# Performance work log

Measured on AMD Instinct MI355X. Metric: run time of the kernel, lower is better.

Reference implementation:

```python
import jax, jax.numpy as jnp
import numpy as np

R_MIN = 0.01
R_MAX = 0.6
H = 32            # polar radial bins (after pooling)
W = 64            # polar angular bins (after pooling)
UP_R = 10         # radial upsampling factor
UP_T = 10         # angular upsampling factor
ATT_ALPHA = 5.0
B, C, IMG = 64, 3, 224


def _conv(x, w, b):
    # NCHW valid conv, stride 1 (matches nn.Conv2d default padding=0)
    y = jax.lax.conv_general_dilated(x, w, (1, 1), 'VALID',
                                     dimension_numbers=('NCHW', 'OIHW', 'NCHW'))
    return y + b[None, :, None, None]


def _maxpool2(x):
    return jax.lax.reduce_window(x, -jnp.inf, jax.lax.max,
                                 (1, 1, 2, 2), (1, 1, 2, 2), 'VALID')


def _grid_sample_border(x, grid):
    # F.grid_sample, bilinear, padding_mode='border', align_corners=False
    Bn, Cn, Hi, Wi = x.shape
    ix = ((grid[..., 0] + 1.0) * Wi - 1.0) * 0.5   # x-coord -> width index
    iy = ((grid[..., 1] + 1.0) * Hi - 1.0) * 0.5   # y-coord -> height index
    x0f = jnp.floor(ix)
    y0f = jnp.floor(iy)
    wx = (ix - x0f)[..., None]
    wy = (iy - y0f)[..., None]
    x0 = jnp.clip(x0f.astype(jnp.int32), 0, Wi - 1)
    x1 = jnp.clip(x0f.astype(jnp.int32) + 1, 0, Wi - 1)
    y0 = jnp.clip(y0f.astype(jnp.int32), 0, Hi - 1)
    y1 = jnp.clip(y0f.astype(jnp.int32) + 1, 0, Hi - 1)
    bidx = jnp.arange(Bn)[:, None, None]
    v00 = x[bidx, :, y0, x0]   # [B,Hg,Wg,C]
    v01 = x[bidx, :, y0, x1]
    v10 = x[bidx, :, y1, x0]
    v11 = x[bidx, :, y1, x1]
    out = (v00 * (1 - wx) * (1 - wy) + v01 * wx * (1 - wy)
           + v10 * (1 - wx) * wy + v11 * wx * wy)
    return jnp.transpose(out, (0, 3, 1, 2))  # [B,C,Hg,Wg]


def setup_inputs() -> dict:
    key = jax.random.key(0)
    ks = jax.random.split(key, 10)
    x = jax.random.normal(ks[0], (B, C, IMG, IMG), dtype=jnp.float32)
    l_t_prev = jax.random.uniform(ks[1], (B, 2), dtype=jnp.float32)
    conv1_w = jax.random.normal(ks[2], (6, C, 5, 5), dtype=jnp.float32) * 0.1
    conv1_b = jnp.zeros((6,), jnp.float32)
    conv2_w = jax.random.normal(ks[3], (16, 6, 5, 5), dtype=jnp.float32) * 0.1
    conv2_b = jnp.zeros((16,), jnp.float32)
    fc1_w = jax.random.normal(ks[4], (8, 16), dtype=jnp.float32) * 0.1
    fc1_b = jnp.zeros((8,), jnp.float32)
    fc2_w = jax.random.normal(ks[5], (2, 8), dtype=jnp.float32) * 0.1
    fc2_b = jnp.zeros((2,), jnp.float32)
    return dict(x=x, l_t_prev=l_t_prev, conv1_w=conv1_w, conv1_b=conv1_b,
                conv2_w=conv2_w, conv2_b=conv2_b, fc1_w=fc1_w, fc1_b=fc1_b,
                fc2_w=fc2_w, fc2_b=fc2_b)


def reference(x, l_t_prev, conv1_w, conv1_b, conv2_w, conv2_b,
              fc1_w, fc1_b, fc2_w, fc2_b):
    # --- attention branch: conv -> maxpool -> conv -> GAP -> fc -> sigmoid ---
    h = _conv(x, conv1_w, conv1_b)
    h = _maxpool2(h)
    h = _conv(h, conv2_w, conv2_b)
    feat = h.mean(axis=(2, 3))                     # AdaptiveAvgPool2d(1), [B,16]
    h = jax.nn.relu(feat @ fc1_w.T + fc1_b)
    weight = jax.nn.sigmoid(h @ fc2_w.T + fc2_b) * ATT_ALPHA   # [B,2]
    # --- per-batch log-polar grid ---
    Hg, Wg = H * UP_R, W * UP_T
    angle = 2.0 * jnp.pi * jnp.arange(Wg, dtype=jnp.float32) / Wg
    unit = jnp.stack([jnp.sin(angle), jnp.cos(angle)], axis=-1)   # [Wg,2]
    start = jnp.log(R_MIN * weight[:, 0])
    stop = jnp.log(R_MAX * weight[:, 1])
    t = jnp.arange(Hg, dtype=jnp.float32) / (Hg - 1)
    radii = jnp.exp(start[:, None] + (stop - start)[:, None] * t[None])  # [B,Hg]
    grid = radii[:, :, None, None] * unit[None, None]     # [B,Hg,Wg,2]
    grid = grid + l_t_prev[:, None, None, :]
    # --- irregular bilinear sampling + box filter ---
    sampled = _grid_sample_border(x, grid)                 # [B,C,Hg,Wg]
    Bn, Cn = sampled.shape[:2]
    pooled = sampled.reshape(Bn, Cn, H, UP_R, W, UP_T).mean(axis=(3, 5))
    return pooled, weight
```

## Files before the change

kernel.cpp:

```cpp
#include <hip/hip_runtime.h>
#include <math.h>

#define Bn    64
#define Cn    3
#define IMG   224
#define PLANE (IMG*IMG)
#define C1    6
#define P1    110
#define P2    106
#define NVALID (P2*P2)
#define Hh    32
#define Ww    64
#define UPR   10
#define UPT   10
#define Hg    (Hh*UPR)
#define Wg    (Ww*UPT)
#define POOLED_SIZE (Bn*Cn*Hh*Ww)
#define RPB   4
#define NCHUNK ((P1 + RPB - 1) / RPB)
#define PSTRIDE 152

typedef unsigned short u16;
typedef float v2f __attribute__((ext_vector_type(2)));

#define PART_FLOATS ((size_t)Bn * NCHUNK * PSTRIDE)
#define X4B_U16     ((size_t)Bn * PLANE * 4)
#define WS_NEEDED   ((PART_FLOATS + Bn * 2) * 4 + X4B_U16 * 2)

__device__ __forceinline__ u16 f2bf(float f) {
    union { unsigned int u; float f; } c; c.f = f;
    unsigned int r = c.u + 0x7fffu + ((c.u >> 16) & 1u);
    return (u16)(r >> 16);
}
__device__ __forceinline__ float bf2f(u16 v) {
    union { unsigned int u; float f; } c; c.u = ((unsigned int)v) << 16;
    return c.f;
}

__device__ __forceinline__ void load_pairs(v2f* P, const float* rp) {
    const float4 a = *(const float4*)rp;
    const float4 c = *(const float4*)(rp + 4);
    P[0] = (v2f){a.x, a.y};
    P[1] = (v2f){a.y, a.z};
    P[2] = (v2f){a.z, a.w};
    P[3] = (v2f){a.w, c.x};
    P[4] = (v2f){c.x, c.y};
    P[5] = (v2f){c.y, c.z};
    P[6] = (v2f){c.z, c.w};
}

__global__ __launch_bounds__(256) void k1_fused(
    const float* __restrict__ x,
    const float* __restrict__ w1,
    const float* __restrict__ b1,
    float* __restrict__ partial,
    u16* __restrict__ x4b,
    int do_pack)
{
    __shared__ __attribute__((aligned(16))) float xs[3][12][224];
    __shared__ float psum[RPB][PSTRIDE];

    const int b    = blockIdx.y;
    const int tid  = threadIdx.x;
    const int wid  = tid >> 6;
    const int lane = tid & 63;

    const float* xb = x + (size_t)b * (Cn * PLANE);

    for (int half = 0; half < 2; ++half) {
        const int chunk = 2 * blockIdx.x + half;
        const int y0 = chunk * RPB;
        const int gybase = 2 * y0;

        for (int i = tid; i < 3 * 12 * 56; i += 256) {
            const int ic  = i / (12 * 56);
            const int rem = i - ic * (12 * 56);
            const int r   = rem / 56;
            const int c4  = rem - r * 56;
            const int gy  = gybase + r;
            if (gy < IMG)
                *(float4*)(&xs[ic][r][c4 * 4]) =
                    *(const float4*)(xb + ic * PLANE + gy * IMG + c4 * 4);
        }
        __syncthreads();

        if (do_pack) {
            u16* ob = x4b + (size_t)b * PLANE * 4;
            for (int i = tid; i < 8 * IMG; i += 256) {
                const int r   = i / IMG;
                const int col = i - r * IMG;
                const int gy  = gybase + r;
                ushort4 v;
                v.x = f2bf(xs[0][r][col]);
                v.y = f2bf(xs[1][r][col]);
                v.z = f2bf(xs[2][r][col]);
                v.w = 0;
                *(ushort4*)(ob + ((size_t)gy * IMG + col) * 4) = v;
            }
        }

        const int y = y0 + wid;
        const bool rowvalid = (y < P1);
        const bool active = (lane < 55) && rowvalid;

        float pp0[C1], pp1[C1];
        if (active) {
            v2f accT01[C1], accT23[C1], accB01[C1], accB23[C1];
            #pragma unroll
            for (int oc = 0; oc < C1; ++oc) {
                const float bv = b1[oc];
                const v2f bvv = (v2f){bv, bv};
                accT01[oc] = bvv; accT23[oc] = bvv;
                accB01[oc] = bvv; accB23[oc] = bvv;
            }

            #pragma unroll
            for (int ic = 0; ic < 3; ++ic) {
                v2f Pa[7], Pb[7];
                load_pairs(Pa, &xs[ic][2 * wid][4 * lane]);
                load_pairs(Pb, &xs[ic][2 * wid + 1][4 * lane]);
                #pragma unroll
                for (int ky = 0; ky < 5; ++ky) {
                    const v2f* Pt = (ky & 1) ? Pb : Pa;
                    const v2f* Po = (ky & 1) ? Pa : Pb;
                    #pragma unroll
                    for (int oc = 0; oc < C1; ++oc) {
                        const float* wrow = w1 + ((oc * 3 + ic) * 25 + ky * 5);
                        #pragma unroll
                        for (int kx = 0; kx < 5; ++kx) {
                            const float wv = wrow[kx];
                            const v2f wvv = (v2f){wv, wv};
                            accT01[oc] += Pt[kx]     * wvv;
                            accT23[oc] += Pt[kx + 2] * wvv;
                            accB01[oc] += Po[kx]     * wvv;
                            accB23[oc] += Po[kx + 2] * wvv;
                        }
                    }
                    if (ky < 4)
                        load_pairs((ky & 1) ? Pb : Pa,
                                   &xs[ic][2 * wid + ky + 2][4 * lane]);
                }
            }

            #pragma unroll
            for (int oc = 0; oc < C1; ++oc) {
                pp0[oc] = fmaxf(fmaxf(accT01[oc].x, accT01[oc].y),
                                fmaxf(accB01[oc].x, accB01[oc].y));
                pp1[oc] = fmaxf(fmaxf(accT23[oc].x, accT23[oc].y),
                                fmaxf(accB23[oc].x, accB23[oc].y));
            }
        } else {
            #pragma unroll
            for (int oc = 0; oc < C1; ++oc) { pp0[oc] = 0.0f; pp1[oc] = 0.0f; }
        }

        #pragma unroll
        for (int oc = 0; oc < C1; ++oc) {
            float s = pp0[oc] + pp1[oc];
            #pragma unroll
            for (int off = 32; off > 0; off >>= 1) s += __shfl_xor(s, off, 64);
            const float c0   = __shfl(pp0[oc], 0, 64);
            const float c1   = __shfl(pp1[oc], 0, 64);
            const float c2   = __shfl(pp0[oc], 1, 64);
            const float c3   = __shfl(pp1[oc], 1, 64);
            const float c106 = __shfl(pp0[oc], 53, 64);
            const float c107 = __shfl(pp1[oc], 53, 64);
            const float c108 = __shfl(pp0[oc], 54, 64);
            const float c109 = __shfl(pp1[oc], 54, 64);
            const float w0v = s - (c106 + c107 + c108 + c109);
            const float w1v = s - c0 - (c107 + c108 + c109);
            const float w2v = s - (c0 + c1) - (c108 + c109);
            const float w3v = s - (c0 + c1 + c2) - c109;
            const float w4v = s - (c0 + c1 + c2 + c3);
            if (lane < 25) {
                const int ky = lane / 5;
                const int kx = lane % 5;
                float wv = w0v;
                wv = (kx == 1) ? w1v : wv;
                wv = (kx == 2) ? w2v : wv;
                wv = (kx == 3) ? w3v : wv;
                wv = (kx == 4) ? w4v : wv;
                const bool valid = rowvalid && ((unsigned)(y - ky) <= 105u);
                psum[wid][oc * 25 + lane] = valid ? wv : 0.0f;
            }
        }
        __syncthreads();

        if (tid < 150) {
            const float v = psum[0][tid] + psum[1][tid] + psum[2][tid] + psum[3][tid];
            partial[((size_t)b * NCHUNK + chunk) * PSTRIDE + tid] = v;
        }
    }
}

__global__ __launch_bounds__(256) void k2_head(
    const float* __restrict__ partial, const float* __restrict__ w2,
    const float* __restrict__ b2, const float* __restrict__ fc1w,
    const float* __restrict__ fc1b, const float* __restrict__ fc2w,
    const float* __restrict__ fc2b, float* __restrict__ wt_ws,
    float* __restrict__ out)
{
    const int b = blockIdx.x;
    const int tid = threadIdx.x;
    __shared__ float wsb[150];
    __shared__ float sfeat[16];
    __shared__ float sh[8];

    if (tid < 150) {
        const float* p = partial + (size_t)b * NCHUNK * PSTRIDE + tid;
        float s = 0.0f;
        #pragma unroll
        for (int c = 0; c < NCHUNK; ++c) s += p[c * PSTRIDE];
        wsb[tid] = s;
    }
    __syncthreads();
    if (tid < 16) {
        float s = 0.0f;
        for (int j = 0; j < 150; ++j) s += w2[tid * 150 + j] * wsb[j];
        sfeat[tid] = b2[tid] + s * (1.0f / (float)NVALID);
    }
    __syncthreads();
    if (tid < 8) {
        float s = fc1b[tid];
        #pragma unroll
        for (int j = 0; j < 16; ++j) s += fc1w[tid * 16 + j] * sfeat[j];
        sh[tid] = fmaxf(s, 0.0f);
    }
    __syncthreads();
    if (tid < 2) {
        float s = fc2b[tid];
        #pragma unroll
        for (int j = 0; j < 8; ++j) s += fc2w[tid * 8 + j] * sh[j];
        float sig = (s >= 0.0f) ? (1.0f / (1.0f + expf(-s)))
                                : (expf(s) / (1.0f + expf(s)));
        const float wgt = 5.0f * sig;
        wt_ws[b * 2 + tid] = wgt;
        out[POOLED_SIZE + b * 2 + tid] = wgt;
    }
}

__device__ __forceinline__ void sample_coords(
    float gxn, float gyn, int& x0, int& y0, float& wx, float& wy)
{
    float ix = ((gxn + 1.0f) * (float)IMG - 1.0f) * 0.5f;
    float iy = ((gyn + 1.0f) * (float)IMG - 1.0f) * 0.5f;
    ix = fminf(fmaxf(ix, 0.0f), (float)(IMG - 1));
    iy = fminf(fmaxf(iy, 0.0f), (float)(IMG - 1));
    x0 = (int)ix; if (x0 > IMG - 2) x0 = IMG - 2;
    y0 = (int)iy; if (y0 > IMG - 2) y0 = IMG - 2;
    wx = ix - (float)x0;
    wy = iy - (float)y0;
}

__global__ __launch_bounds__(640) void k3_sample_pool_bf16(
    const u16* __restrict__ x4b,
    const float* __restrict__ ltp,
    const float* __restrict__ wt,
    float* __restrict__ out)
{
    __shared__ float part[3 * Wg];

    const int L = blockIdx.x;
    const int q = L >> 3;
    const int h = q & 31;
    const int b = (L & 7) + 8 * (q >> 5);
    const int tid = threadIdx.x;

    const float w0 = wt[b * 2 + 0];
    const float w1 = wt[b * 2 + 1];
    const float l0 = ltp[b * 2 + 0];
    const float l1 = ltp[b * 2 + 1];
    const float start = logf(0.01f * w0);
    const float stop  = logf(0.6f  * w1);
    const float dr = stop - start;

    const float angle = 6.283185307179586f * (float)tid / (float)Wg;
    const float sn = sinf(angle);
    const float cs = cosf(angle);

    const u16* xb4 = x4b + (size_t)b * PLANE * 4;

    const float ratio = expf(dr * (1.0f / (float)(Hg - 1)));
    float r = expf(start + dr * ((float)(h * UPR) / (float)(Hg - 1)));

    float acc0 = 0.0f, acc1 = 0.0f, acc2 = 0.0f;
    #pragma unroll
    for (int i = 0; i < UPR; ++i) {
        int x0, y0; float wx, wy;
        sample_coords(r * sn + l0, r * cs + l1, x0, y0, wx, wy);
        r *= ratio;

        const u16* base = xb4 + ((size_t)(y0 * IMG + x0)) * 4;
        const ushort4 a00 = *(const ushort4*)(base);
        const ushort4 a01 = *(const ushort4*)(base + 4);
        const ushort4 a10 = *(const ushort4*)(base + IMG * 4);
        const ushort4 a11 = *(const ushort4*)(base + IMG * 4 + 4);

        const float wx0 = 1.0f - wx, wy0 = 1.0f - wy;
        const float w00 = wx0 * wy0, w01 = wx * wy0;
        const float w10 = wx0 * wy,  w11 = wx * wy;

        acc0 += w00*bf2f(a00.x) + w01*bf2f(a01.x) + w10*bf2f(a10.x) + w11*bf2f(a11.x);
        acc1 += w00*bf2f(a00.y) + w01*bf2f(a01.y) + w10*bf2f(a10.y) + w11*bf2f(a11.y);
        acc2 += w00*bf2f(a00.z) + w01*bf2f(a01.z) + w10*bf2f(a10.z) + w11*bf2f(a11.z);
    }
    part[0 * Wg + tid] = acc0;
    part[1 * Wg + tid] = acc1;
    part[2 * Wg + tid] = acc2;
    __syncthreads();

    if (tid < Cn * Ww) {
        const int c = tid / Ww;
        const int w = tid % Ww;
        const float* p = part + c * Wg + w * UPT;
        float s = 0.0f;
        #pragma unroll
        for (int j = 0; j < UPT; ++j) s += p[j];
        out[(((size_t)b * Cn + c) * Hh + h) * Ww + w] = s * (1.0f / (UPR * UPT));
    }
}

__global__ __launch_bounds__(640) void k3_sample_pool_nchw(
    const float* __restrict__ x, const float* __restrict__ ltp,
    const float* __restrict__ wt, float* __restrict__ out)
{
    __shared__ float part[3 * Wg];
    const int L = blockIdx.x;
    const int q = L >> 3;
    const int h = q & 31;
    const int b = (L & 7) + 8 * (q >> 5);
    const int tid = threadIdx.x;

    const float w0 = wt[b * 2 + 0];
    const float w1 = wt[b * 2 + 1];
    const float l0 = ltp[b * 2 + 0];
    const float l1 = ltp[b * 2 + 1];
    const float start = logf(0.01f * w0);
    const float stop  = logf(0.6f  * w1);
    const float dr = stop - start;
    const float angle = 6.283185307179586f * (float)tid / (float)Wg;
    const float sn = sinf(angle);
    const float cs = cosf(angle);
    const float* xb = x + (size_t)b * Cn * PLANE;

    const float ratio = expf(dr * (1.0f / (float)(Hg - 1)));
    float r = expf(start + dr * ((float)(h * UPR) / (float)(Hg - 1)));

    float acc0 = 0.0f, acc1 = 0.0f, acc2 = 0.0f;
    #pragma unroll
    for (int i = 0; i < UPR; ++i) {
        int x0, y0; float wx, wy;
        sample_coords(r * sn + l0, r * cs + l1, x0, y0, wx, wy);
        r *= ratio;
        const float wx0 = 1.0f - wx, wy0 = 1.0f - wy;
        const float w00 = wx0 * wy0, w01 = wx * wy0;
        const float w10 = wx0 * wy,  w11 = wx * wy;
        const int o00 = y0 * IMG + x0;
        acc0 += w00*xb[o00] + w01*xb[o00+1] + w10*xb[o00+IMG] + w11*xb[o00+IMG+1];
        const float* x1p = xb + PLANE;
        acc1 += w00*x1p[o00] + w01*x1p[o00+1] + w10*x1p[o00+IMG] + w11*x1p[o00+IMG+1];
        const float* x2p = xb + 2 * PLANE;
        acc2 += w00*x2p[o00] + w01*x2p[o00+1] + w10*x2p[o00+IMG] + w11*x2p[o00+IMG+1];
    }
    part[0 * Wg + tid] = acc0;
    part[1 * Wg + tid] = acc1;
    part[2 * Wg + tid] = acc2;
    __syncthreads();

    if (tid < Cn * Ww) {
        const int c = tid / Ww;
        const int w = tid % Ww;
        const float* p = part + c * Wg + w * UPT;
        float s = 0.0f;
        #pragma unroll
        for (int j = 0; j < UPT; ++j) s += p[j];
        out[(((size_t)b * Cn + c) * Hh + h) * Ww + w] = s * (1.0f / (UPR * UPT));
    }
}

extern "C" void kernel_launch(void* const* d_in, const int* in_sizes, int n_in,
                              void* d_out, int out_size, void* d_ws, size_t ws_size,
                              hipStream_t stream) {
    const float* x       = (const float*)d_in[0];
    const float* ltp     = (const float*)d_in[1];
    const float* conv1_w = (const float*)d_in[2];
    const float* conv1_b = (const float*)d_in[3];
    const float* conv2_w = (const float*)d_in[4];
    const float* conv2_b = (const float*)d_in[5];
    const float* fc1_w   = (const float*)d_in[6];
    const float* fc1_b   = (const float*)d_in[7];
    const float* fc2_w   = (const float*)d_in[8];
    const float* fc2_b   = (const float*)d_in[9];
    float* out = (float*)d_out;

    const int do_pack = (ws_size >= WS_NEEDED) ? 1 : 0;

    float* part_ws = (float*)d_ws;
    float* wt_ws   = part_ws + PART_FLOATS;
    u16*   x4b     = (u16*)(wt_ws + Bn * 2);

    k1_fused<<<dim3(NCHUNK / 2, Bn), dim3(256), 0, stream>>>(
        x, conv1_w, conv1_b, part_ws, x4b, do_pack);
    k2_head<<<dim3(Bn), dim3(256), 0, stream>>>(part_ws, conv2_w, conv2_b,
                                                fc1_w, fc1_b, fc2_w, fc2_b,
                                                wt_ws, out);
    if (do_pack)
        k3_sample_pool_bf16<<<dim3(Hh * Bn), dim3(Wg), 0, stream>>>(x4b, ltp, wt_ws, out);
    else
        k3_sample_pool_nchw<<<dim3(Hh * Bn), dim3(Wg), 0, stream>>>(x, ltp, wt_ws, out);
}
```

Baseline: 176.4 us.

## Compute conv1 with bf16 MFMA using hi/lo weight split

Rewrites the first convolution + maxpool stage to run on MFMA 16x16x32 bf16 matrix instructions instead of scalar FMA. Input is converted to packed bf16 in shared memory, and weights are split into hi and lo bf16 parts to keep near-fp32 accuracy for the weights, though inputs are rounded to bf16. Each block now handles one 8-row chunk with 28 chunks per batch, and the pooled column sums and edge corrections are reorganised for the new layout. The goal is to cut the ALU cost of the conv, which dominates k1. The risk is the precision loss from bf16 inputs plus extra reduction complexity.

```diff
diff --git a/kernel.cpp b/kernel.cpp
--- a/kernel.cpp
+++ b/kernel.cpp
@@ -16,12 +16,13 @@
 #define Hg    (Hh*UPR)
 #define Wg    (Ww*UPT)
 #define POOLED_SIZE (Bn*Cn*Hh*Ww)
-#define RPB   4
-#define NCHUNK ((P1 + RPB - 1) / RPB)
+#define NCHUNK 28
 #define PSTRIDE 152
+#define ROWB  (IMG*8)
 
 typedef unsigned short u16;
-typedef float v2f __attribute__((ext_vector_type(2)));
+typedef short s8v __attribute__((ext_vector_type(8)));
+typedef float f4v __attribute__((ext_vector_type(4)));
 
 #define PART_FLOATS ((size_t)Bn * NCHUNK * PSTRIDE)
 #define X4B_U16     ((size_t)Bn * PLANE * 4)
@@ -37,17 +38,7 @@
     return c.f;
 }
 
-__device__ __forceinline__ void load_pairs(v2f* P, const float* rp) {
-    const float4 a = *(const float4*)rp;
-    const float4 c = *(const float4*)(rp + 4);
-    P[0] = (v2f){a.x, a.y};
-    P[1] = (v2f){a.y, a.z};
-    P[2] = (v2f){a.z, a.w};
-    P[3] = (v2f){a.w, c.x};
-    P[4] = (v2f){c.x, c.y};
-    P[5] = (v2f){c.y, c.z};
-    P[6] = (v2f){c.z, c.w};
-}
+#define GSHFL(v, idx) __shfl((v), (lane & 48) + (idx), 64)
 
 __global__ __launch_bounds__(256) void k1_fused(
     const float* __restrict__ x,
@@ -57,139 +48,159 @@
     u16* __restrict__ x4b,
     int do_pack)
 {
-    __shared__ __attribute__((aligned(16))) float xs[3][12][224];
-    __shared__ float psum[RPB][PSTRIDE];
-
-    const int b    = blockIdx.y;
-    const int tid  = threadIdx.x;
-    const int wid  = tid >> 6;
-    const int lane = tid & 63;
+    __shared__ __attribute__((aligned(16))) unsigned char xs[12 * ROWB + 128];
+    __shared__ float rowR[4][C1][4];
+    __shared__ float edgeLo[4][C1][4];
+    __shared__ float edgeHi[4][C1][4];
+
+    const int b     = blockIdx.y;
+    const int chunk = blockIdx.x;
+    const int tid   = threadIdx.x;
+    const int wid   = tid >> 6;
+    const int lane  = tid & 63;
+    const int n     = lane & 15;
+    const int g     = lane >> 4;
+    const int gy0   = chunk * 8;
 
     const float* xb = x + (size_t)b * (Cn * PLANE);
 
-    for (int half = 0; half < 2; ++half) {
-        const int chunk = 2 * blockIdx.x + half;
-        const int y0 = chunk * RPB;
-        const int gybase = 2 * y0;
-
-        for (int i = tid; i < 3 * 12 * 56; i += 256) {
-            const int ic  = i / (12 * 56);
-            const int rem = i - ic * (12 * 56);
-            const int r   = rem / 56;
-            const int c4  = rem - r * 56;
-            const int gy  = gybase + r;
-            if (gy < IMG)
-                *(float4*)(&xs[ic][r][c4 * 4]) =
-                    *(const float4*)(xb + ic * PLANE + gy * IMG + c4 * 4);
-        }
-        __syncthreads();
-
-        if (do_pack) {
-            u16* ob = x4b + (size_t)b * PLANE * 4;
-            for (int i = tid; i < 8 * IMG; i += 256) {
-                const int r   = i / IMG;
-                const int col = i - r * IMG;
-                const int gy  = gybase + r;
-                ushort4 v;
-                v.x = f2bf(xs[0][r][col]);
-                v.y = f2bf(xs[1][r][col]);
-                v.z = f2bf(xs[2][r][col]);
-                v.w = 0;
-                *(ushort4*)(ob + ((size_t)gy * IMG + col) * 4) = v;
+    s8v ahi[5], alo[5];
+    #pragma unroll
+    for (int ky = 0; ky < 5; ++ky) {
+        #pragma unroll
+        for (int j = 0; j < 8; ++j) {
+            const int kmem = g * 8 + j;
+            const int ic = kmem & 3, kx = kmem >> 2;
+            float w = 0.0f;
+            if (n < C1 && ic < 3 && kx < 5)
+                w = w1[((n * 3 + ic) * 5 + ky) * 5 + kx];
+            const u16 hb = f2bf(w);
+            ahi[ky][j] = (short)hb;
+            alo[ky][j] = (short)f2bf(w - bf2f(hb));
+        }
+    }
+    f4v binit;
+    #pragma unroll
+    for (int e = 0; e < 4; ++e) {
+        const int oc = g * 4 + e;
+        binit[e] = (oc < C1) ? b1[oc] : 0.0f;
+    }
+
+    u16* ob = x4b + (size_t)b * PLANE * 4;
+    for (int i = tid; i < 12 * 112; i += 256) {
+        const int r = i / 112;
+        const int p = i - r * 112;
+        const int gy = gy0 + r;
+        uint4 U; U.x = U.y = U.z = U.w = 0u;
+        if (gy < IMG) {
+            const float2 v0 = *(const float2*)(xb + 0 * PLANE + gy * IMG + 2 * p);
+            const float2 v1 = *(const float2*)(xb + 1 * PLANE + gy * IMG + 2 * p);
+            const float2 v2 = *(const float2*)(xb + 2 * PLANE + gy * IMG + 2 * p);
+            U.x = (unsigned)f2bf(v0.x) | ((unsigned)f2bf(v1.x) << 16);
+            U.y = (unsigned)f2bf(v2.x);
+            U.z = (unsigned)f2bf(v0.y) | ((unsigned)f2bf(v1.y) << 16);
+            U.w = (unsigned)f2bf(v2.y);
+        }
+        *(uint4*)(xs + r * ROWB + p * 16) = U;
+        if (do_pack && r < 8)
+            *(uint4*)(ob + ((size_t)gy * IMG + 2 * p) * 4) = U;
+    }
+    __syncthreads();
+
+    float colsum[4][4];
+    #pragma unroll
+    for (int py = 0; py < 4; ++py)
+        #pragma unroll
+        for (int e = 0; e < 4; ++e) colsum[py][e] = 0.0f;
+
+    for (int si = 0; si < 4; ++si) {
+        const int s = wid + 4 * si;
+        if (s >= 14) break;
+        const unsigned sByte = (unsigned)(s * 128 + n * 8 + g * 16);
+
+        f4v acc[8];
+        #pragma unroll
+        for (int q = 0; q < 8; ++q) acc[q] = binit;
+
+        #pragma unroll
+        for (int r = 0; r < 12; ++r) {
+            s8v bf;
+            const unsigned char* bp = xs + r * ROWB + sByte;
+            ((unsigned long long*)&bf)[0] = *(const unsigned long long*)bp;
+            ((unsigned long long*)&bf)[1] = *(const unsigned long long*)(bp + 8);
+            #pragma unroll
+            for (int ky = 0; ky < 5; ++ky) {
+                const int q = r - ky;
+                if (q >= 0 && q < 8)
+                    acc[q] = __builtin_amdgcn_mfma_f32_16x16x32_bf16(
+                        ahi[ky], bf, acc[q], 0, 0, 0);
             }
-        }
-
-        const int y = y0 + wid;
-        const bool rowvalid = (y < P1);
-        const bool active = (lane < 55) && rowvalid;
-
-        float pp0[C1], pp1[C1];
-        if (active) {
-            v2f accT01[C1], accT23[C1], accB01[C1], accB23[C1];
             #pragma unroll
-            for (int oc = 0; oc < C1; ++oc) {
-                const float bv = b1[oc];
-                const v2f bvv = (v2f){bv, bv};
-                accT01[oc] = bvv; accT23[oc] = bvv;
-                accB01[oc] = bvv; accB23[oc] = bvv;
+            for (int ky = 0; ky < 5; ++ky) {
+                const int q = r - ky;
+                if (q >= 0 && q < 8)
+                    acc[q] = __builtin_amdgcn_mfma_f32_16x16x32_bf16(
+                        alo[ky], bf, acc[q], 0, 0, 0);
             }
-
+        }
+
+        #pragma unroll
+        for (int py = 0; py < 4; ++py) {
             #pragma unroll
-            for (int ic = 0; ic < 3; ++ic) {
-                v2f Pa[7], Pb[7];
-                load_pairs(Pa, &xs[ic][2 * wid][4 * lane]);
-                load_pairs(Pb, &xs[ic][2 * wid + 1][4 * lane]);
-                #pragma unroll
-                for (int ky = 0; ky < 5; ++ky) {
-                    const v2f* Pt = (ky & 1) ? Pb : Pa;
-                    const v2f* Po = (ky & 1) ? Pa : Pb;
-                    #pragma unroll
-                    for (int oc = 0; oc < C1; ++oc) {
-                        const float* wrow = w1 + ((oc * 3 + ic) * 25 + ky * 5);
-                        #pragma unroll
-                        for (int kx = 0; kx < 5; ++kx) {
-                            const float wv = wrow[kx];
-                            const v2f wvv = (v2f){wv, wv};
-                            accT01[oc] += Pt[kx]     * wvv;
-                            accT23[oc] += Pt[kx + 2] * wvv;
-                            accB01[oc] += Po[kx]     * wvv;
-                            accB23[oc] += Po[kx + 2] * wvv;
-                        }
-                    }
-                    if (ky < 4)
-                        load_pairs((ky & 1) ? Pb : Pa,
-                                   &xs[ic][2 * wid + ky + 2][4 * lane]);
+            for (int e = 0; e < 4; ++e) {
+                float t = fmaxf(acc[2 * py][e], acc[2 * py + 1][e]);
+                t = fmaxf(t, __shfl_xor(t, 1, 64));
+                if (s == 13 && n >= 12) t = 0.0f;
+                colsum[py][e] += t;
+                const int oc = g * 4 + e;
+                if (s == 0) {
+                    const float c0 = GSHFL(t, 0), c1 = GSHFL(t, 2);
+                    const float c2 = GSHFL(t, 4), c3 = GSHFL(t, 6);
+                    const float S1 = c0, S2 = S1 + c1, S3 = S2 + c2, S4 = S3 + c3;
+                    const float sv = (n == 0) ? S1 : (n == 1) ? S2 : (n == 2) ? S3 : S4;
+                    if (n < 4 && oc < C1) edgeLo[py][oc][n] = sv;
+                }
+                if (s == 13) {
+                    const float d109 = GSHFL(t, 10), d108 = GSHFL(t, 8);
+                    const float d107 = GSHFL(t, 6),  d106 = GSHFL(t, 4);
+                    const float U1 = d109, U2 = U1 + d108, U3 = U2 + d107, U4 = U3 + d106;
+                    const float uv = (n == 0) ? U1 : (n == 1) ? U2 : (n == 2) ? U3 : U4;
+                    if (n < 4 && oc < C1) edgeHi[py][oc][n] = uv;
                 }
             }
-
-            #pragma unroll
-            for (int oc = 0; oc < C1; ++oc) {
-                pp0[oc] = fmaxf(fmaxf(accT01[oc].x, accT01[oc].y),
-                                fmaxf(accB01[oc].x, accB01[oc].y));
-                pp1[oc] = fmaxf(fmaxf(accT23[oc].x, accT23[oc].y),
-                                fmaxf(accB23[oc].x, accB23[oc].y));
-            }
-        } else {
-            #pragma unroll
-            for (int oc = 0; oc < C1; ++oc) { pp0[oc] = 0.0f; pp1[oc] = 0.0f; }
-        }
-
-        #pragma unroll
-        for (int oc = 0; oc < C1; ++oc) {
-            float s = pp0[oc] + pp1[oc];
-            #pragma unroll
-            for (int off = 32; off > 0; off >>= 1) s += __shfl_xor(s, off, 64);
-            const float c0   = __shfl(pp0[oc], 0, 64);
-            const float c1   = __shfl(pp1[oc], 0, 64);
-            const float c2   = __shfl(pp0[oc], 1, 64);
-            const float c3   = __shfl(pp1[oc], 1, 64);
-            const float c106 = __shfl(pp0[oc], 53, 64);
-            const float c107 = __shfl(pp1[oc], 53, 64);
-            const float c108 = __shfl(pp0[oc], 54, 64);
-            const float c109 = __shfl(pp1[oc], 54, 64);
-            const float w0v = s - (c106 + c107 + c108 + c109);
-            const float w1v = s - c0 - (c107 + c108 + c109);
-            const float w2v = s - (c0 + c1) - (c108 + c109);
-            const float w3v = s - (c0 + c1 + c2) - c109;
-            const float w4v = s - (c0 + c1 + c2 + c3);
-            if (lane < 25) {
-                const int ky = lane / 5;
-                const int kx = lane % 5;
-                float wv = w0v;
-                wv = (kx == 1) ? w1v : wv;
-                wv = (kx == 2) ? w2v : wv;
-                wv = (kx == 3) ? w3v : wv;
-                wv = (kx == 4) ? w4v : wv;
-                const bool valid = rowvalid && ((unsigned)(y - ky) <= 105u);
-                psum[wid][oc * 25 + lane] = valid ? wv : 0.0f;
-            }
-        }
-        __syncthreads();
-
-        if (tid < 150) {
-            const float v = psum[0][tid] + psum[1][tid] + psum[2][tid] + psum[3][tid];
-            partial[((size_t)b * NCHUNK + chunk) * PSTRIDE + tid] = v;
-        }
+        }
+    }
+
+    #pragma unroll
+    for (int py = 0; py < 4; ++py) {
+        #pragma unroll
+        for (int e = 0; e < 4; ++e) {
+            float v = colsum[py][e];
+            v += __shfl_xor(v, 2, 64);
+            v += __shfl_xor(v, 4, 64);
+            v += __shfl_xor(v, 8, 64);
+            const int oc = g * 4 + e;
+            if (n == 0 && oc < C1) rowR[wid][oc][py] = v;
+        }
+    }
+    __syncthreads();
+
+    if (tid < 150) {
+        const int oc = tid / 25;
+        const int rem = tid - oc * 25;
+        const int ky = rem / 5, kx = rem - ky * 5;
+        float total = 0.0f;
+        #pragma unroll
+        for (int py = 0; py < 4; ++py) {
+            const int y = chunk * 4 + py;
+            const bool valid = (y < P1) && ((unsigned)(y - ky) <= 105u);
+            float v = rowR[0][oc][py] + rowR[1][oc][py]
+                    + rowR[2][oc][py] + rowR[3][oc][py];
+            if (kx > 0) v -= edgeLo[py][oc][kx - 1];
+            if (kx < 4) v -= edgeHi[py][oc][3 - kx];
+            total += valid ? v : 0.0f;
+        }
+        partial[((size_t)b * NCHUNK + chunk) * PSTRIDE + tid] = total;
     }
 }
 
@@ -399,7 +410,7 @@
     float* wt_ws   = part_ws + PART_FLOATS;
     u16*   x4b     = (u16*)(wt_ws + Bn * 2);
 
-    k1_fused<<<dim3(NCHUNK / 2, Bn), dim3(256), 0, stream>>>(
+    k1_fused<<<dim3(NCHUNK, Bn), dim3(256), 0, stream>>>(
         x, conv1_w, conv1_b, part_ws, x4b, do_pack);
     k2_head<<<dim3(Bn), dim3(256), 0, stream>>>(part_ws, conv2_w, conv2_b,
                                                 fc1_w, fc1_b, fc2_w, fc2_b,
```

After: 175.7 us. Within noise of the previous version (-0.4%).
